# Kernel optimization log

Measured on AMD Instinct MI355X. Metric: run time of the kernel, lower is better.

Reference implementation:

```python
import jax, jax.numpy as jnp
import numpy as np

B, S, D = 8, 2048, 256
EXP = 4
NEG = -1e9
EPS = 1e-5


def layer_norm(x, w, b):
    mu = jnp.mean(x, axis=-1, keepdims=True)
    var = jnp.var(x, axis=-1, keepdims=True)
    return (x - mu) * jax.lax.rsqrt(var + EPS) * w + b


def setup_inputs() -> dict:
    key = jax.random.key(0)
    ks = jax.random.split(key, 8)
    x = jax.random.normal(ks[0], (B, S, D), dtype=jnp.float32)
    r_mat = jax.random.normal(ks[1], (B, S, S), dtype=jnp.float32)
    attn_mask = jax.random.randint(ks[2], (S, S), 0, 2).astype(jnp.float32)
    pad_mask = jax.random.randint(ks[3], (B, 1, S), 0, 2).astype(jnp.float32)
    w1 = jax.random.normal(ks[4], (D, EXP * D), dtype=jnp.float32) / np.sqrt(D)
    b1 = jnp.zeros((EXP * D,), dtype=jnp.float32)
    w2 = jax.random.normal(ks[5], (EXP * D, D), dtype=jnp.float32) / np.sqrt(EXP * D)
    b2 = jnp.zeros((D,), dtype=jnp.float32)
    ln1_w = jnp.ones((D,), dtype=jnp.float32)
    ln1_b = jnp.zeros((D,), dtype=jnp.float32)
    ln2_w = jnp.ones((D,), dtype=jnp.float32)
    ln2_b = jnp.zeros((D,), dtype=jnp.float32)
    return {"x": x, "r_mat": r_mat, "attn_mask": attn_mask, "pad_mask": pad_mask,
            "ln1_w": ln1_w, "ln1_b": ln1_b, "ln2_w": ln2_w, "ln2_b": ln2_b,
            "w1": w1, "b1": b1, "w2": w2, "b2": b2}


def reference(x, r_mat, attn_mask, pad_mask, ln1_w, ln1_b, ln2_w, ln2_b, w1, b1, w2, b2):
    # sublayer 0: pre-LN + InrAwaSA + residual
    h = layer_norm(x, ln1_w, ln1_b)                       # [B,S,D]
    scale = jnp.sqrt(jnp.float32(D))
    scores = jnp.einsum("bqd,bkd->bqk", h, h) / scale      # [B,S,S]
    # mask r_mat by pad_mask [B,1,S] and attn_mask [1,S,S], then softmax
    rm = jnp.where(pad_mask == 0.0, NEG, r_mat)
    rm = jnp.where(attn_mask[None] == 0.0, NEG, rm)
    scores = scores + jax.nn.softmax(rm, axis=-1)
    # NOTE: the torch source calls scores.masked_fill(...) non-in-place and
    # discards the result, so scores are NOT re-masked here (faithful no-op).
    prob = jax.nn.softmax(scores, axis=-1)
    x = x + jnp.einsum("bqk,bkd->bqd", prob, h)
    # sublayer 1: pre-LN + FFN + residual (dropout is identity in eval)
    h2 = layer_norm(x, ln2_w, ln2_b)
    ffn = jax.nn.relu(h2 @ w1 + b1) @ w2 + b2
    return x + ffn
```

## Files before the change

kernel.cpp:

```cpp
#include <hip/hip_runtime.h>
#include <stdint.h>

#define NB 8
#define SS 2048
#define DD 256
#define NEGV -1e9f
#define LDSW 136

typedef __attribute__((ext_vector_type(8))) __bf16 bf16x8;
typedef __attribute__((ext_vector_type(4))) float f32x4;

union U16 { uint4 u; bf16x8 b; unsigned short us[8]; };

__device__ __forceinline__ unsigned short tobf(float v) {
  union { float f; uint32_t u; } c; c.f = v;
  uint32_t r = (c.u + 0x7fffu + ((c.u >> 16) & 1u)) >> 16;
  return (unsigned short)r;
}
__device__ __forceinline__ float frombf(unsigned short v) {
  union { uint32_t u; float f; } c; c.u = ((uint32_t)v) << 16;
  return c.f;
}

__device__ __forceinline__ void glds16(const unsigned short* g, unsigned short* l) {
  __builtin_amdgcn_global_load_lds(
      (const __attribute__((address_space(1))) uint32_t*)g,
      (__attribute__((address_space(3))) uint32_t*)l, 16, 0, 0);
}

__device__ __forceinline__ void stage_tile(const unsigned short* src, int ld,
                                           unsigned short* lbuf, int w, int lane) {
  int rl = lane >> 2;
  int cs = (lane & 3) * 8;
  glds16(src + (size_t)(w * 32 + rl) * ld + cs, lbuf + w * 1024);
  glds16(src + (size_t)(w * 32 + 16 + rl) * ld + cs, lbuf + w * 1024 + 512);
}

template <int NSTEPS>
__device__ __forceinline__ void gemm128_tile(
    const unsigned short* __restrict__ A, int lda,
    const unsigned short* __restrict__ Bt, int ldb,
    unsigned short* smem, f32x4 (&acc)[4][4]) {
  unsigned short* lA = smem;
  unsigned short* lB = smem + 8192;
  const int w = threadIdx.x >> 6, lane = threadIdx.x & 63;
  const int lr = lane & 15, lg = lane >> 4;
  const int wm = w >> 1, wn = w & 1;
#pragma unroll
  for (int i = 0; i < 4; ++i)
#pragma unroll
    for (int j = 0; j < 4; ++j) acc[i][j] = (f32x4){0.f, 0.f, 0.f, 0.f};
  stage_tile(A, lda, lA, w, lane);
  stage_tile(Bt, ldb, lB, w, lane);
  __syncthreads();
  for (int s = 0; s < NSTEPS; ++s) {
    const unsigned short* cA = lA + (s & 1) * 4096;
    const unsigned short* cB = lB + (s & 1) * 4096;
    if (s + 1 < NSTEPS) {
      stage_tile(A + (s + 1) * 32, lda, lA + ((s + 1) & 1) * 4096, w, lane);
      stage_tile(Bt + (s + 1) * 32, ldb, lB + ((s + 1) & 1) * 4096, w, lane);
    }
    bf16x8 am[4], bn[4];
#pragma unroll
    for (int i = 0; i < 4; ++i) {
      U16 u; u.u = *(const uint4*)(cA + (wm * 64 + i * 16 + lr) * 32 + lg * 8);
      am[i] = u.b;
      U16 v; v.u = *(const uint4*)(cB + (wn * 64 + i * 16 + lr) * 32 + lg * 8);
      bn[i] = v.b;
    }
#pragma unroll
    for (int i = 0; i < 4; ++i)
#pragma unroll
      for (int j = 0; j < 4; ++j)
        acc[i][j] = __builtin_amdgcn_mfma_f32_16x16x32_bf16(am[i], bn[j], acc[i][j], 0, 0, 0);
    __syncthreads();
  }
}

__global__ void ln_kernel(const float* __restrict__ in, const float* __restrict__ w,
                          const float* __restrict__ bparm, unsigned short* __restrict__ outb) {
  int row = blockIdx.x * 4 + (threadIdx.x >> 6);
  int lane = threadIdx.x & 63;
  const float* xr = in + (size_t)row * DD;
  float4 v = *(const float4*)(xr + lane * 4);
  float s = v.x + v.y + v.z + v.w;
  float s2 = v.x * v.x + v.y * v.y + v.z * v.z + v.w * v.w;
#pragma unroll
  for (int m = 1; m < 64; m <<= 1) { s += __shfl_xor(s, m); s2 += __shfl_xor(s2, m); }
  float mu = s * (1.f / DD);
  float var = s2 * (1.f / DD) - mu * mu;
  float rs = rsqrtf(var + 1e-5f);
  float4 wv = *(const float4*)(w + lane * 4);
  float4 bv = *(const float4*)(bparm + lane * 4);
  ushort4 o;
  o.x = tobf((v.x - mu) * rs * wv.x + bv.x);
  o.y = tobf((v.y - mu) * rs * wv.y + bv.y);
  o.z = tobf((v.z - mu) * rs * wv.z + bv.z);
  o.w = tobf((v.w - mu) * rs * wv.w + bv.w);
  *(ushort4*)(outb + (size_t)row * DD + lane * 4) = o;
}

__global__ void transpose_kernel(const unsigned short* __restrict__ in,
                                 unsigned short* __restrict__ out) {
  __shared__ unsigned short tile[64][72];
  int bid = blockIdx.x;
  int b = bid >> 7;
  int rest = bid & 127;
  int st = rest >> 2, dt = rest & 3;
  int s0 = st * 64, d0 = dt * 64;
  int t = threadIdx.x;
  int r = t >> 2, cs = (t & 3) * 16;
  const unsigned short* src = in + ((size_t)b * SS + s0 + r) * DD + d0 + cs;
  *(uint4*)&tile[r][cs] = *(const uint4*)src;
  *(uint4*)&tile[r][cs + 8] = *(const uint4*)(src + 8);
  __syncthreads();
  union { unsigned short us[16]; uint4 u[2]; } tmp;
  int dr = t >> 2, sseg = (t & 3) * 16;
#pragma unroll
  for (int j = 0; j < 16; ++j) tmp.us[j] = tile[sseg + j][dr];
  unsigned short* dst = out + ((size_t)b * DD + d0 + dr) * SS + s0 + sseg;
  *(uint4*)dst = tmp.u[0];
  *(uint4*)(dst + 8) = tmp.u[1];
}

__global__ __launch_bounds__(256) void qk_kernel(
    const unsigned short* __restrict__ hb,
    unsigned short* __restrict__ S) {
  __shared__ unsigned short smem[17408];
  int bid = blockIdx.x;
  int b = bid & 7;
  int t = bid >> 3;
  int mb = 0, rem = t;
  while (rem >= 16 - mb) { rem -= 16 - mb; ++mb; }
  int nb = mb + rem;
  const unsigned short* A = hb + (size_t)(b * SS + mb * 128) * DD;
  const unsigned short* Bt = hb + (size_t)(b * SS + nb * 128) * DD;
  f32x4 acc[4][4];
  gemm128_tile<8>(A, DD, Bt, DD, smem, acc);
  int tid = threadIdx.x;
  int w = tid >> 6, lane = tid & 63;
  int lr = lane & 15, lg = lane >> 4;
  int wm = w >> 1, wn = w & 1;
  unsigned short* Sb = S + (size_t)b * SS * SS;
#pragma unroll
  for (int i = 0; i < 4; ++i)
#pragma unroll
    for (int j = 0; j < 4; ++j)
#pragma unroll
      for (int r = 0; r < 4; ++r) {
        int m = mb * 128 + wm * 64 + i * 16 + lg * 4 + r;
        int n = nb * 128 + wn * 64 + j * 16 + lr;
        Sb[(size_t)m * SS + n] = tobf(acc[i][j][r] * 0.0625f);
      }
  if (mb != nb) {
#pragma unroll
    for (int i = 0; i < 4; ++i)
#pragma unroll
      for (int j = 0; j < 4; ++j) {
        int col = wn * 64 + j * 16 + lr;
#pragma unroll
        for (int r = 0; r < 4; ++r) {
          int row = wm * 64 + i * 16 + lg * 4 + r;
          smem[col * LDSW + row] = tobf(acc[i][j][r] * 0.0625f);
        }
      }
    __syncthreads();
    int row2 = tid >> 1, half = (tid & 1) * 64;
    const unsigned short* s = smem + row2 * LDSW + half;
    unsigned short* d = Sb + (size_t)(nb * 128 + row2) * SS + mb * 128 + half;
    uint4 vv[8];
#pragma unroll
    for (int k = 0; k < 8; ++k) vv[k] = *(const uint4*)(s + k * 8);
#pragma unroll
    for (int k = 0; k < 8; ++k) *(uint4*)(d + k * 8) = vv[k];
  }
}

__global__ __launch_bounds__(256) void smfuse_kernel(
    const float* __restrict__ r_mat,
    const float* __restrict__ attn,
    const float* __restrict__ pad,
    unsigned short* __restrict__ S) {
  int row = blockIdx.x * 4 + (threadIdx.x >> 6);
  int lane = threadIdx.x & 63;
  int b = row >> 11, q = row & 2047;
  const float* rrow = r_mat + (size_t)row * SS;
  const float* arow = attn + (size_t)q * SS;
  const float* prow = pad + (size_t)b * SS;
  unsigned short* srow = S + (size_t)row * SS;

  float rm[32];
  float mx = -__builtin_inff();
#pragma unroll
  for (int i = 0; i < 8; ++i) {
    int c = i * 256 + lane * 4;
    float4 rv = *(const float4*)(rrow + c);
    float4 av = *(const float4*)(arow + c);
    float4 pv = *(const float4*)(prow + c);
    float v0 = (pv.x == 0.f || av.x == 0.f) ? NEGV : rv.x;
    float v1 = (pv.y == 0.f || av.y == 0.f) ? NEGV : rv.y;
    float v2 = (pv.z == 0.f || av.z == 0.f) ? NEGV : rv.z;
    float v3 = (pv.w == 0.f || av.w == 0.f) ? NEGV : rv.w;
    rm[i * 4 + 0] = v0; rm[i * 4 + 1] = v1; rm[i * 4 + 2] = v2; rm[i * 4 + 3] = v3;
    mx = fmaxf(mx, fmaxf(fmaxf(v0, v1), fmaxf(v2, v3)));
  }
#pragma unroll
  for (int m = 1; m < 64; m <<= 1) mx = fmaxf(mx, __shfl_xor(mx, m));
  float sum = 0.f;
#pragma unroll
  for (int j = 0; j < 32; ++j) { rm[j] = __expf(rm[j] - mx); sum += rm[j]; }
#pragma unroll
  for (int m = 1; m < 64; m <<= 1) sum += __shfl_xor(sum, m);
  float inv = 1.f / sum;

  float sc[32];
  float mx2 = -__builtin_inff();
#pragma unroll
  for (int i = 0; i < 8; ++i) {
    int c = i * 256 + lane * 4;
    ushort4 sv = *(const ushort4*)(srow + c);
    float s0 = frombf(sv.x) + rm[i * 4 + 0] * inv;
    float s1 = frombf(sv.y) + rm[i * 4 + 1] * inv;
    float s2 = frombf(sv.z) + rm[i * 4 + 2] * inv;
    float s3 = frombf(sv.w) + rm[i * 4 + 3] * inv;
    sc[i * 4 + 0] = s0; sc[i * 4 + 1] = s1; sc[i * 4 + 2] = s2; sc[i * 4 + 3] = s3;
    mx2 = fmaxf(mx2, fmaxf(fmaxf(s0, s1), fmaxf(s2, s3)));
  }
#pragma unroll
  for (int m = 1; m < 64; m <<= 1) mx2 = fmaxf(mx2, __shfl_xor(mx2, m));
  float sum2 = 0.f;
#pragma unroll
  for (int j = 0; j < 32; ++j) { sc[j] = __expf(sc[j] - mx2); sum2 += sc[j]; }
#pragma unroll
  for (int m = 1; m < 64; m <<= 1) sum2 += __shfl_xor(sum2, m);
  float inv2 = 1.f / sum2;
#pragma unroll
  for (int i = 0; i < 8; ++i) {
    int c = i * 256 + lane * 4;
    ushort4 o;
    o.x = tobf(sc[i * 4 + 0] * inv2);
    o.y = tobf(sc[i * 4 + 1] * inv2);
    o.z = tobf(sc[i * 4 + 2] * inv2);
    o.w = tobf(sc[i * 4 + 3] * inv2);
    *(ushort4*)(srow + c) = o;
  }
}

__global__ __launch_bounds__(256) void pv_kernel(
    const unsigned short* __restrict__ P,
    const unsigned short* __restrict__ hbT,
    unsigned short* __restrict__ pvp) {
  __shared__ unsigned short smem[16384];
  int bid = blockIdx.x;
  int b = bid & 7;
  int rest = bid >> 3;
  int ks = rest & 3;
  int rest2 = rest >> 2;
  int nb = rest2 & 1, mb = rest2 >> 1;
  const unsigned short* A = P + (size_t)(b * SS + mb * 128) * SS + ks * 512;
  const unsigned short* Bt = hbT + (size_t)(b * DD + nb * 128) * SS + ks * 512;
  f32x4 acc[4][4];
  gemm128_tile<16>(A, SS, Bt, SS, smem, acc);
  int w = threadIdx.x >> 6, lane = threadIdx.x & 63;
  int lr = lane & 15, lg = lane >> 4;
  int wm = w >> 1, wn = w & 1;
  unsigned short* O = pvp + ((size_t)(ks << 14) + (b << 11) + mb * 128) * DD + nb * 128;
#pragma unroll
  for (int i = 0; i < 4; ++i)
#pragma unroll
    for (int j = 0; j < 4; ++j)
#pragma unroll
      for (int r = 0; r < 4; ++r) {
        int m = wm * 64 + i * 16 + lg * 4 + r;
        int n = wn * 64 + j * 16 + lr;
        O[(size_t)m * DD + n] = tobf(acc[i][j][r]);
      }
}

__global__ __launch_bounds__(256) void pvreduce_kernel(
    const unsigned short* __restrict__ pvp,
    const float* __restrict__ x,
    const float* __restrict__ ln2w,
    const float* __restrict__ ln2b,
    float* __restrict__ out,
    unsigned short* __restrict__ h2b) {
  int r = blockIdx.x * 4 + (threadIdx.x >> 6);
  int lane = threadIdx.x & 63;
  int c = lane * 4;
  float o[4] = {0.f, 0.f, 0.f, 0.f};
#pragma unroll
  for (int ks = 0; ks < 4; ++ks) {
    ushort4 pk = *(const ushort4*)(pvp + ((size_t)(ks << 14) + r) * DD + c);
    o[0] += frombf(pk.x); o[1] += frombf(pk.y);
    o[2] += frombf(pk.z); o[3] += frombf(pk.w);
  }
  float4 xv = *(const float4*)(x + (size_t)r * DD + c);
  float val[4] = {o[0] + xv.x, o[1] + xv.y, o[2] + xv.z, o[3] + xv.w};
  float4 ov = {val[0], val[1], val[2], val[3]};
  *(float4*)(out + (size_t)r * DD + c) = ov;
  float s = val[0] + val[1] + val[2] + val[3];
  float s2 = val[0] * val[0] + val[1] * val[1] + val[2] * val[2] + val[3] * val[3];
#pragma unroll
  for (int m = 1; m < 64; m <<= 1) { s += __shfl_xor(s, m); s2 += __shfl_xor(s2, m); }
  float mu = s * (1.f / DD);
  float var = s2 * (1.f / DD) - mu * mu;
  float rsv = rsqrtf(var + 1e-5f);
  float4 wv = *(const float4*)(ln2w + c);
  float4 bv = *(const float4*)(ln2b + c);
  ushort4 h;
  h.x = tobf((val[0] - mu) * rsv * wv.x + bv.x);
  h.y = tobf((val[1] - mu) * rsv * wv.y + bv.y);
  h.z = tobf((val[2] - mu) * rsv * wv.z + bv.z);
  h.w = tobf((val[3] - mu) * rsv * wv.w + bv.w);
  *(ushort4*)(h2b + (size_t)r * DD + c) = h;
}

__global__ void wconv_kernel(const float* __restrict__ w1, unsigned short* __restrict__ w1bT,
                             const float* __restrict__ w2, unsigned short* __restrict__ w2bT) {
  __shared__ unsigned short tile[64][72];
  int bid = blockIdx.x;
  const float* src; unsigned short* dst; int K, N, t;
  if (bid < 64) { src = w1; dst = w1bT; K = 256; N = 1024; t = bid; }
  else          { src = w2; dst = w2bT; K = 1024; N = 256; t = bid - 64; }
  int nt = N >> 6;
  int kt = t / nt, ntb = t % nt;
  int k0 = kt * 64, n0 = ntb * 64;
  int tt = threadIdx.x;
  int r = tt >> 2, c4 = (tt & 3) * 16;
  const float* s = src + (size_t)(k0 + r) * N + n0 + c4;
#pragma unroll
  for (int j = 0; j < 16; ++j) tile[r][c4 + j] = tobf(s[j]);
  __syncthreads();
  union { unsigned short us[16]; uint4 u[2]; } tmp;
  int nr = tt >> 2, ks = (tt & 3) * 16;
#pragma unroll
  for (int j = 0; j < 16; ++j) tmp.us[j] = tile[ks + j][nr];
  unsigned short* d = dst + (size_t)(n0 + nr) * K + k0 + ks;
  *(uint4*)d = tmp.u[0];
  *(uint4*)(d + 8) = tmp.u[1];
}

__global__ __launch_bounds__(256) void ffn1_kernel(
    const unsigned short* __restrict__ A0,
    const unsigned short* __restrict__ Bt0,
    const float* __restrict__ bias,
    unsigned short* __restrict__ Out) {
  __shared__ unsigned short smem[16384];
  int bid = blockIdx.x;
  int nb = bid & 7, mb = bid >> 3;
  const unsigned short* A = A0 + (size_t)(mb * 128) * 256;
  const unsigned short* Bt = Bt0 + (size_t)(nb * 128) * 256;
  f32x4 acc[4][4];
  gemm128_tile<8>(A, 256, Bt, 256, smem, acc);
  int w = threadIdx.x >> 6, lane = threadIdx.x & 63;
  int lr = lane & 15, lg = lane >> 4;
  int wm = w >> 1, wn = w & 1;
#pragma unroll
  for (int i = 0; i < 4; ++i)
#pragma unroll
    for (int j = 0; j < 4; ++j)
#pragma unroll
      for (int r = 0; r < 4; ++r) {
        int m = mb * 128 + wm * 64 + i * 16 + lg * 4 + r;
        int n = nb * 128 + wn * 64 + j * 16 + lr;
        float v = fmaxf(acc[i][j][r] + bias[n], 0.f);
        Out[(size_t)m * 1024 + n] = tobf(v);
      }
}

__global__ __launch_bounds__(256) void ffn2_kernel(
    const unsigned short* __restrict__ A0,
    const unsigned short* __restrict__ Bt0,
    unsigned short* __restrict__ f2p) {
  __shared__ unsigned short smem[16384];
  int bid = blockIdx.x;
  int ks = bid & 3;
  int rest = bid >> 2;
  int nb = rest & 1, mb = rest >> 1;
  const unsigned short* A = A0 + (size_t)(mb * 128) * 1024 + ks * 256;
  const unsigned short* Bt = Bt0 + (size_t)(nb * 128) * 1024 + ks * 256;
  f32x4 acc[4][4];
  gemm128_tile<8>(A, 1024, Bt, 1024, smem, acc);
  int w = threadIdx.x >> 6, lane = threadIdx.x & 63;
  int lr = lane & 15, lg = lane >> 4;
  int wm = w >> 1, wn = w & 1;
  unsigned short* O = f2p + (size_t)(ks << 14) * DD;
#pragma unroll
  for (int i = 0; i < 4; ++i)
#pragma unroll
    for (int j = 0; j < 4; ++j)
#pragma unroll
      for (int r = 0; r < 4; ++r) {
        int m = mb * 128 + wm * 64 + i * 16 + lg * 4 + r;
        int n = nb * 128 + wn * 64 + j * 16 + lr;
        O[(size_t)m * DD + n] = tobf(acc[i][j][r]);
      }
}

__global__ __launch_bounds__(256) void f2reduce_kernel(
    const unsigned short* __restrict__ f2p,
    const float* __restrict__ bias,
    float* __restrict__ out) {
  int r = blockIdx.x * 4 + (threadIdx.x >> 6);
  int lane = threadIdx.x & 63;
  int c = lane * 4;
  float o[4] = {0.f, 0.f, 0.f, 0.f};
#pragma unroll
  for (int ks = 0; ks < 4; ++ks) {
    ushort4 pk = *(const ushort4*)(f2p + ((size_t)(ks << 14) + r) * DD + c);
    o[0] += frombf(pk.x); o[1] += frombf(pk.y);
    o[2] += frombf(pk.z); o[3] += frombf(pk.w);
  }
  float4 bv = *(const float4*)(bias + c);
  float* orow = out + (size_t)r * DD + c;
  float4 cur = *(const float4*)orow;
  float4 res = {cur.x + o[0] + bv.x, cur.y + o[1] + bv.y,
                cur.z + o[2] + bv.z, cur.w + o[3] + bv.w};
  *(float4*)orow = res;
}

extern "C" void kernel_launch(void* const* d_in, const int* in_sizes, int n_in,
                              void* d_out, int out_size, void* d_ws, size_t ws_size,
                              hipStream_t stream) {
  const float* x     = (const float*)d_in[0];
  const float* r_mat = (const float*)d_in[1];
  const float* attn  = (const float*)d_in[2];
  const float* pad   = (const float*)d_in[3];
  const float* ln1w  = (const float*)d_in[4];
  const float* ln1b  = (const float*)d_in[5];
  const float* ln2w  = (const float*)d_in[6];
  const float* ln2b  = (const float*)d_in[7];
  const float* w1    = (const float*)d_in[8];
  const float* b1    = (const float*)d_in[9];
  const float* w2    = (const float*)d_in[10];
  const float* b2    = (const float*)d_in[11];
  float* out = (float*)d_out;

  uint8_t* ws = (uint8_t*)d_ws;
  unsigned short* hb   = (unsigned short*)(ws + 0);
  unsigned short* hbT  = (unsigned short*)(ws + 8388608);
  unsigned short* h2b  = (unsigned short*)(ws + 16777216);
  unsigned short* w1bT = (unsigned short*)(ws + 25165824);
  unsigned short* w2bT = (unsigned short*)(ws + 25690112);
  unsigned short* S    = (unsigned short*)(ws + 33554432);
  unsigned short* pvp  = (unsigned short*)(ws + 100663296);
  unsigned short* t    = S;
  unsigned short* f2p  = pvp;

  hipLaunchKernelGGL(ln_kernel, dim3(4096), dim3(256), 0, stream, x, ln1w, ln1b, hb);
  hipLaunchKernelGGL(transpose_kernel, dim3(1024), dim3(256), 0, stream, hb, hbT);
  hipLaunchKernelGGL(qk_kernel, dim3(1088), dim3(256), 0, stream, hb, S);
  hipLaunchKernelGGL(smfuse_kernel, dim3(4096), dim3(256), 0, stream, r_mat, attn, pad, S);
  hipLaunchKernelGGL(pv_kernel, dim3(1024), dim3(256), 0, stream, S, hbT, pvp);
  hipLaunchKernelGGL(pvreduce_kernel, dim3(4096), dim3(256), 0, stream,
                     pvp, x, ln2w, ln2b, out, h2b);
  hipLaunchKernelGGL(wconv_kernel, dim3(128), dim3(256), 0, stream, w1, w1bT, w2, w2bT);
  hipLaunchKernelGGL(ffn1_kernel, dim3(1024), dim3(256), 0, stream, h2b, w1bT, b1, t);
  hipLaunchKernelGGL(ffn2_kernel, dim3(1024), dim3(256), 0, stream, t, w2bT, f2p);
  hipLaunchKernelGGL(f2reduce_kernel, dim3(4096), dim3(256), 0, stream, f2p, b2, out);
}
```

Baseline: 196.4 us.

## Widen PV and FFN GEMM tiles to 128x256 with 8-wave blocks

Measured after the change: 186.0 us. -5.3%, faster.

```diff
diff --git a/kernel.cpp b/kernel.cpp
--- a/kernel.cpp
+++ b/kernel.cpp
@@ -59,6 +59,54 @@
     if (s + 1 < NSTEPS) {
       stage_tile(A + (s + 1) * 32, lda, lA + ((s + 1) & 1) * 4096, w, lane);
       stage_tile(Bt + (s + 1) * 32, ldb, lB + ((s + 1) & 1) * 4096, w, lane);
+    }
+    bf16x8 am[4], bn[4];
+#pragma unroll
+    for (int i = 0; i < 4; ++i) {
+      U16 u; u.u = *(const uint4*)(cA + (wm * 64 + i * 16 + lr) * 32 + lg * 8);
+      am[i] = u.b;
+      U16 v; v.u = *(const uint4*)(cB + (wn * 64 + i * 16 + lr) * 32 + lg * 8);
+      bn[i] = v.b;
+    }
+#pragma unroll
+    for (int i = 0; i < 4; ++i)
+#pragma unroll
+      for (int j = 0; j < 4; ++j)
+        acc[i][j] = __builtin_amdgcn_mfma_f32_16x16x32_bf16(am[i], bn[j], acc[i][j], 0, 0, 0);
+    __syncthreads();
+  }
+}
+
+template <int NSTEPS>
+__device__ __forceinline__ void gemm256_acc(
+    const unsigned short* __restrict__ A, int lda,
+    const unsigned short* __restrict__ Bt, int ldb,
+    unsigned short* smem, f32x4 (&acc)[4][4]) {
+  unsigned short* lA = smem;
+  unsigned short* lB = smem + 8192;
+  const int tid = threadIdx.x;
+  const int w = tid >> 6, lane = tid & 63;
+  const int lr = lane & 15, lg = lane >> 4;
+  const int wm = w >> 2, wn = w & 3;
+  const int rl = lane >> 2, cs = (lane & 3) * 8;
+#pragma unroll
+  for (int i = 0; i < 4; ++i)
+#pragma unroll
+    for (int j = 0; j < 4; ++j) acc[i][j] = (f32x4){0.f, 0.f, 0.f, 0.f};
+  glds16(A + (size_t)(w * 16 + rl) * lda + cs, lA + w * 512);
+  glds16(Bt + (size_t)(w * 32 + rl) * ldb + cs, lB + w * 1024);
+  glds16(Bt + (size_t)(w * 32 + 16 + rl) * ldb + cs, lB + w * 1024 + 512);
+  __syncthreads();
+  for (int s = 0; s < NSTEPS; ++s) {
+    const unsigned short* cA = lA + (s & 1) * 4096;
+    const unsigned short* cB = lB + (s & 1) * 8192;
+    if (s + 1 < NSTEPS) {
+      const unsigned short* An = A + (s + 1) * 32;
+      const unsigned short* Bn = Bt + (s + 1) * 32;
+      glds16(An + (size_t)(w * 16 + rl) * lda + cs, lA + ((s + 1) & 1) * 4096 + w * 512);
+      glds16(Bn + (size_t)(w * 32 + rl) * ldb + cs, lB + ((s + 1) & 1) * 8192 + w * 1024);
+      glds16(Bn + (size_t)(w * 32 + 16 + rl) * ldb + cs,
+             lB + ((s + 1) & 1) * 8192 + w * 1024 + 512);
     }
     bf16x8 am[4], bn[4];
 #pragma unroll
@@ -246,25 +294,23 @@
   }
 }
 
-__global__ __launch_bounds__(256) void pv_kernel(
+__global__ __launch_bounds__(512) void pv_kernel(
     const unsigned short* __restrict__ P,
     const unsigned short* __restrict__ hbT,
     unsigned short* __restrict__ pvp) {
-  __shared__ unsigned short smem[16384];
+  __shared__ unsigned short smem[24576];
   int bid = blockIdx.x;
   int b = bid & 7;
   int rest = bid >> 3;
-  int ks = rest & 3;
-  int rest2 = rest >> 2;
-  int nb = rest2 & 1, mb = rest2 >> 1;
+  int ks = rest & 3, mb = rest >> 2;
   const unsigned short* A = P + (size_t)(b * SS + mb * 128) * SS + ks * 512;
-  const unsigned short* Bt = hbT + (size_t)(b * DD + nb * 128) * SS + ks * 512;
+  const unsigned short* Bt = hbT + (size_t)(b * DD) * SS + ks * 512;
   f32x4 acc[4][4];
-  gemm128_tile<16>(A, SS, Bt, SS, smem, acc);
+  gemm256_acc<16>(A, SS, Bt, SS, smem, acc);
   int w = threadIdx.x >> 6, lane = threadIdx.x & 63;
   int lr = lane & 15, lg = lane >> 4;
-  int wm = w >> 1, wn = w & 1;
-  unsigned short* O = pvp + ((size_t)(ks << 14) + (b << 11) + mb * 128) * DD + nb * 128;
+  int wm = w >> 2, wn = w & 3;
+  unsigned short* O = pvp + ((size_t)(ks << 14) + (b << 11) + mb * 128) * DD;
 #pragma unroll
   for (int i = 0; i < 4; ++i)
 #pragma unroll
@@ -340,21 +386,21 @@
   *(uint4*)(d + 8) = tmp.u[1];
 }
 
-__global__ __launch_bounds__(256) void ffn1_kernel(
+__global__ __launch_bounds__(512) void ffn1_kernel(
     const unsigned short* __restrict__ A0,
     const unsigned short* __restrict__ Bt0,
     const float* __restrict__ bias,
     unsigned short* __restrict__ Out) {
-  __shared__ unsigned short smem[16384];
+  __shared__ unsigned short smem[24576];
   int bid = blockIdx.x;
-  int nb = bid & 7, mb = bid >> 3;
+  int nb = bid & 3, mb = bid >> 2;
   const unsigned short* A = A0 + (size_t)(mb * 128) * 256;
-  const unsigned short* Bt = Bt0 + (size_t)(nb * 128) * 256;
+  const unsigned short* Bt = Bt0 + (size_t)(nb * 256) * 256;
   f32x4 acc[4][4];
-  gemm128_tile<8>(A, 256, Bt, 256, smem, acc);
+  gemm256_acc<8>(A, 256, Bt, 256, smem, acc);
   int w = threadIdx.x >> 6, lane = threadIdx.x & 63;
   int lr = lane & 15, lg = lane >> 4;
-  int wm = w >> 1, wn = w & 1;
+  int wm = w >> 2, wn = w & 3;
 #pragma unroll
   for (int i = 0; i < 4; ++i)
 #pragma unroll
@@ -362,37 +408,35 @@
 #pragma unroll
       for (int r = 0; r < 4; ++r) {
         int m = mb * 128 + wm * 64 + i * 16 + lg * 4 + r;
-        int n = nb * 128 + wn * 64 + j * 16 + lr;
+        int n = nb * 256 + wn * 64 + j * 16 + lr;
         float v = fmaxf(acc[i][j][r] + bias[n], 0.f);
         Out[(size_t)m * 1024 + n] = tobf(v);
       }
 }
 
-__global__ __launch_bounds__(256) void ffn2_kernel(
+__global__ __launch_bounds__(512) void ffn2_kernel(
     const unsigned short* __restrict__ A0,
     const unsigned short* __restrict__ Bt0,
     unsigned short* __restrict__ f2p) {
-  __shared__ unsigned short smem[16384];
+  __shared__ unsigned short smem[24576];
   int bid = blockIdx.x;
-  int ks = bid & 3;
-  int rest = bid >> 2;
-  int nb = rest & 1, mb = rest >> 1;
+  int ks = bid & 3, mb = bid >> 2;
   const unsigned short* A = A0 + (size_t)(mb * 128) * 1024 + ks * 256;
-  const unsigned short* Bt = Bt0 + (size_t)(nb * 128) * 1024 + ks * 256;
+  const unsigned short* Bt = Bt0 + ks * 256;
   f32x4 acc[4][4];
-  gemm128_tile<8>(A, 1024, Bt, 1024, smem, acc);
+  gemm256_acc<8>(A, 1024, Bt, 1024, smem, acc);
   int w = threadIdx.x >> 6, lane = threadIdx.x & 63;
   int lr = lane & 15, lg = lane >> 4;
-  int wm = w >> 1, wn = w & 1;
-  unsigned short* O = f2p + (size_t)(ks << 14) * DD;
+  int wm = w >> 2, wn = w & 3;
+  unsigned short* O = f2p + ((size_t)(ks << 14) + mb * 128) * DD;
 #pragma unroll
   for (int i = 0; i < 4; ++i)
 #pragma unroll
     for (int j = 0; j < 4; ++j)
 #pragma unroll
       for (int r = 0; r < 4; ++r) {
-        int m = mb * 128 + wm * 64 + i * 16 + lg * 4 + r;
-        int n = nb * 128 + wn * 64 + j * 16 + lr;
+        int m = wm * 64 + i * 16 + lg * 4 + r;
+        int n = wn * 64 + j * 16 + lr;
         O[(size_t)m * DD + n] = tobf(acc[i][j][r]);
       }
 }
@@ -451,11 +495,11 @@
   hipLaunchKernelGGL(transpose_kernel, dim3(1024), dim3(256), 0, stream, hb, hbT);
   hipLaunchKernelGGL(qk_kernel, dim3(1088), dim3(256), 0, stream, hb, S);
   hipLaunchKernelGGL(smfuse_kernel, dim3(4096), dim3(256), 0, stream, r_mat, attn, pad, S);
-  hipLaunchKernelGGL(pv_kernel, dim3(1024), dim3(256), 0, stream, S, hbT, pvp);
+  hipLaunchKernelGGL(pv_kernel, dim3(512), dim3(512), 0, stream, S, hbT, pvp);
   hipLaunchKernelGGL(pvreduce_kernel, dim3(4096), dim3(256), 0, stream,
                      pvp, x, ln2w, ln2b, out, h2b);
   hipLaunchKernelGGL(wconv_kernel, dim3(128), dim3(256), 0, stream, w1, w1bT, w2, w2bT);
-  hipLaunchKernelGGL(ffn1_kernel, dim3(1024), dim3(256), 0, stream, h2b, w1bT, b1, t);
-  hipLaunchKernelGGL(ffn2_kernel, dim3(1024), dim3(256), 0, stream, t, w2bT, f2p);
+  hipLaunchKernelGGL(ffn1_kernel, dim3(512), dim3(512), 0, stream, h2b, w1bT, b1, t);
+  hipLaunchKernelGGL(ffn2_kernel, dim3(512), dim3(512), 0, stream, t, w2bT, f2p);
   hipLaunchKernelGGL(f2reduce_kernel, dim3(4096), dim3(256), 0, stream, f2p, b2, out);
 }
```
